# Performance work log

Hardware: AMD Instinct MI355X
Metric: run time of the kernel (lower is better)

## Reference

```python
import jax, jax.numpy as jnp
import numpy as np

GROUP = 64   # quantization group size (nunchaku W4A4 default)
QMAX = 7.0   # symmetric int4 positive range


def setup_inputs() -> dict:
    key = jax.random.key(0)
    ks = jax.random.split(key, 6)
    T, K, N, R = 256, 3072, 3072, 32
    x = jax.random.normal(ks[0], (T, K), dtype=jnp.float32)
    # int4 weight codes stored as 0..15 (dequant subtracts zero-point 8)
    qweight = jax.random.randint(ks[1], (N, K), 0, 16, dtype=jnp.int32)
    # per-(out_channel, input_group) weight scales, small positive
    wscales = jax.random.uniform(ks[2], (N, K // GROUP), dtype=jnp.float32) * 0.02 + 1e-3
    lora_down = jax.random.normal(ks[3], (R, K), dtype=jnp.float32) / np.sqrt(K)
    lora_up = jax.random.normal(ks[4], (N, R), dtype=jnp.float32) / np.sqrt(R)
    bias = jax.random.normal(ks[5], (N,), dtype=jnp.float32) * 0.01
    return {"x": x, "qweight": qweight, "wscales": wscales,
            "lora_down": lora_down, "lora_up": lora_up, "bias": bias}


def _quantize_act(x):
    # per-token, per-group symmetric int4 fake-quant (quantize -> dequantize)
    T, K = x.shape
    xg = x.reshape(T, K // GROUP, GROUP)
    scale = jnp.maximum(jnp.max(jnp.abs(xg), axis=-1, keepdims=True) / QMAX, 1e-8)
    q = jnp.clip(jnp.round(xg / scale), -8.0, QMAX)
    return (q * scale).reshape(T, K)


def reference(x, qweight, wscales, lora_down, lora_up, bias):
    # Dequantize int4 weights: (code - 8) * per-group scale  -> [N, K]
    N, K = qweight.shape
    w = (qweight.astype(jnp.float32) - 8.0).reshape(N, K // GROUP, GROUP)
    w = (w * wscales[:, :, None]).reshape(N, K)
    # W4A4 main path: int4-quantized activations x dequantized int4 weights
    x_dq = _quantize_act(x)
    main = x_dq @ w.T                               # [T, N]
    # fused low-rank (SVDQuant LoRA) branch on full-precision activations
    lora = (x @ lora_down.T) @ lora_up.T            # [T, R] @ [R, N]
    return main + lora + bias
```

## Files before the change

kernel.cpp:

```cpp
#include <hip/hip_runtime.h>
#include <stdint.h>

#define T_DIM 256
#define K_DIM 3072
#define N_DIM 3072
#define R_DIM 32
#define KG    48
#define NSPLIT 6

#define QA_BLOCKS 3072
#define LM_BLOCKS 96
#define BO_BLOCKS 768

typedef __bf16 bf16x8 __attribute__((ext_vector_type(8)));
typedef float  f32x4  __attribute__((ext_vector_type(4)));
typedef unsigned short u16x8 __attribute__((ext_vector_type(8)));

__device__ __forceinline__ unsigned short f2bf(float f) {
    unsigned u = __builtin_bit_cast(unsigned, f);
    unsigned rounding = 0x7FFFu + ((u >> 16) & 1u);
    return (unsigned short)((u + rounding) >> 16);
}

__device__ __forceinline__ bf16x8 cvt8(const float* p) {
    float4 lo = ((const float4*)p)[0], hi = ((const float4*)p)[1];
    bf16x8 v;
    v[0] = (__bf16)lo.x; v[1] = (__bf16)lo.y; v[2] = (__bf16)lo.z; v[3] = (__bf16)lo.w;
    v[4] = (__bf16)hi.x; v[5] = (__bf16)hi.y; v[6] = (__bf16)hi.z; v[7] = (__bf16)hi.w;
    return v;
}

__global__ __launch_bounds__(256) void prep(
        const float* __restrict__ x,
        const float* __restrict__ lora_down,
        const float* __restrict__ bias,
        unsigned short* __restrict__ Ap,
        float*          __restrict__ Lm,
        float*          __restrict__ out) {
    int blk = blockIdx.x;
    if (blk < QA_BLOCKS) {
        int widx = blk * 4 + (threadIdx.x >> 6);
        int lane = threadIdx.x & 63;
        int t = widx / KG, g = widx % KG;
        float v = x[(size_t)t * K_DIM + g * 64 + lane];
        float a = fabsf(v);
        #pragma unroll
        for (int off = 32; off; off >>= 1) a = fmaxf(a, __shfl_xor(a, off));
        float scale = fmaxf(a / 7.0f, 1e-8f);
        float q = rintf(v / scale);
        q = fminf(fmaxf(q, -8.f), 7.f);
        Ap[(((size_t)g * 8 + (lane >> 3)) * 256 + t) * 8 + (lane & 7)] = f2bf(q * scale);
    } else if (blk < QA_BLOCKS + LM_BLOCKS) {
        int kb = blk - QA_BLOCKS;
        int lane = threadIdx.x & 63, wv = threadIdx.x >> 6;
        int mrow = lane & 15, quad = lane >> 4;
        int k0 = kb * 32 + quad * 8;
        bf16x8 a[4], b[2];
        #pragma unroll
        for (int mt = 0; mt < 4; ++mt)
            a[mt] = cvt8(x + (size_t)(wv * 64 + mt * 16 + mrow) * K_DIM + k0);
        #pragma unroll
        for (int nt = 0; nt < 2; ++nt)
            b[nt] = cvt8(lora_down + (size_t)(nt * 16 + mrow) * K_DIM + k0);
        f32x4 acc[4][2];
        f32x4 zero = {0.f, 0.f, 0.f, 0.f};
        #pragma unroll
        for (int i = 0; i < 4; ++i) { acc[i][0] = zero; acc[i][1] = zero; }
        #pragma unroll
        for (int mt = 0; mt < 4; ++mt)
            #pragma unroll
            for (int nt = 0; nt < 2; ++nt)
                acc[mt][nt] = __builtin_amdgcn_mfma_f32_16x16x32_bf16(
                    a[mt], b[nt], acc[mt][nt], 0, 0, 0);
        #pragma unroll
        for (int mt = 0; mt < 4; ++mt)
            #pragma unroll
            for (int nt = 0; nt < 2; ++nt)
                #pragma unroll
                for (int r = 0; r < 4; ++r)
                    atomicAdd(&Lm[(size_t)(wv * 64 + mt * 16 + quad * 4 + r) * R_DIM
                                  + nt * 16 + mrow], acc[mt][nt][r]);
    } else {
        int i = (blk - QA_BLOCKS - LM_BLOCKS) * 256 + threadIdx.x;
        float4 bv = *(const float4*)&bias[(i * 4) % N_DIM];
        ((float4*)out)[i] = bv;
    }
}

__global__ __launch_bounds__(256) void gemm_main(
        const uint4*    __restrict__ ApU,
        const int*      __restrict__ qweight,
        const float*    __restrict__ wscales,
        const float*    __restrict__ Lm,
        const float*    __restrict__ lora_up,
        float*          __restrict__ out) {
    __shared__ uint4 BsU[2][512];
    int nblk  = blockIdx.x;
    int mblk  = blockIdx.y;
    int split = blockIdx.z;
    int c0 = split * (KG / NSPLIT);
    int c1 = (split == NSPLIT - 1) ? KG + 1 : c0 + (KG / NSPLIT);
    int tid = threadIdx.x;
    int lane = tid & 63, wv = tid >> 6;
    int mrow = lane & 15, quad = lane >> 4;
    int n_row = tid >> 2, seg = tid & 3;
    const int nbase = nblk * 64;
    const int mbase = mblk * 128 + wv * 32;

    f32x4 acc[2][4];
    f32x4 zero = {0.f, 0.f, 0.f, 0.f};
    #pragma unroll
    for (int i = 0; i < 2; ++i)
        #pragma unroll
        for (int j = 0; j < 4; ++j) acc[i][j] = zero;

    int4  qc[2][4];
    float wsr[2];
    bf16x8 af[2][2][2];

    const float* wsrow = wscales + (size_t)(nbase + n_row) * KG;
    const int4* qrow = (const int4*)(qweight + (size_t)(nbase + n_row) * K_DIM + seg * 16);

    #define AFRAG(kt, ks, mt) \
        (*(const bf16x8*)&ApU[(size_t)(kt) * 2048 + ((ks) * 4 + quad) * 256 + \
                              mbase + (mt) * 16 + mrow])

    {
        #pragma unroll
        for (int ks = 0; ks < 2; ++ks)
            #pragma unroll
            for (int mt = 0; mt < 2; ++mt)
                af[0][ks][mt] = AFRAG(c0, ks, mt);
        #pragma unroll
        for (int j = 0; j < 4; ++j) {
            qc[0][j] = qrow[(size_t)c0 * 16 + j];
            qc[1][j] = qrow[(size_t)(c0 + 1) * 16 + j];
        }
        wsr[0] = wsrow[c0];
        wsr[1] = wsrow[c0 + 1];
    }

    #define STEP(PP, KT)                                                          \
    {                                                                             \
        constexpr int p = (PP);                                                   \
        const int kk = (KT);                                                      \
        if (kk < KG) {                                                            \
            float w = wsr[p];                                                     \
            float m8w = -8.0f * w;                                                \
            int4 ca = qc[p][0], cb = qc[p][1], cc = qc[p][2], cd = qc[p][3];      \
            bf16x8 v0, v1;                                                        \
            v0[0] = (__bf16)__builtin_fmaf((float)ca.x, w, m8w);                  \
            v0[1] = (__bf16)__builtin_fmaf((float)ca.y, w, m8w);                  \
            v0[2] = (__bf16)__builtin_fmaf((float)ca.z, w, m8w);                  \
            v0[3] = (__bf16)__builtin_fmaf((float)ca.w, w, m8w);                  \
            v0[4] = (__bf16)__builtin_fmaf((float)cb.x, w, m8w);                  \
            v0[5] = (__bf16)__builtin_fmaf((float)cb.y, w, m8w);                  \
            v0[6] = (__bf16)__builtin_fmaf((float)cb.z, w, m8w);                  \
            v0[7] = (__bf16)__builtin_fmaf((float)cb.w, w, m8w);                  \
            v1[0] = (__bf16)__builtin_fmaf((float)cc.x, w, m8w);                  \
            v1[1] = (__bf16)__builtin_fmaf((float)cc.y, w, m8w);                  \
            v1[2] = (__bf16)__builtin_fmaf((float)cc.z, w, m8w);                  \
            v1[3] = (__bf16)__builtin_fmaf((float)cc.w, w, m8w);                  \
            v1[4] = (__bf16)__builtin_fmaf((float)cd.x, w, m8w);                  \
            v1[5] = (__bf16)__builtin_fmaf((float)cd.y, w, m8w);                  \
            v1[6] = (__bf16)__builtin_fmaf((float)cd.z, w, m8w);                  \
            v1[7] = (__bf16)__builtin_fmaf((float)cd.w, w, m8w);                  \
            BsU[p][(seg * 2 + 0) * 64 + n_row] = __builtin_bit_cast(uint4, v0);   \
            BsU[p][(seg * 2 + 1) * 64 + n_row] = __builtin_bit_cast(uint4, v1);   \
        } else {                                                                  \
            bf16x8 v0 = __builtin_bit_cast(bf16x8, (u16x8)(0));                   \
            bf16x8 v1 = __builtin_bit_cast(bf16x8, (u16x8)(0));                   \
            if (seg < 2) {                                                        \
                const float* lu = lora_up + (size_t)(nbase + n_row) * R_DIM + seg * 16; \
                _Pragma("unroll")                                                 \
                for (int j = 0; j < 8; ++j) {                                     \
                    v0[j] = (__bf16)lu[j];                                        \
                    v1[j] = (__bf16)lu[8 + j];                                    \
                }                                                                 \
            }                                                                     \
            BsU[p][(seg * 2 + 0) * 64 + n_row] = __builtin_bit_cast(uint4, v0);   \
            BsU[p][(seg * 2 + 1) * 64 + n_row] = __builtin_bit_cast(uint4, v1);   \
        }                                                                         \
        __syncthreads();                                                          \
        if (kk + 2 < c1 && kk + 2 < KG) {                                         \
            _Pragma("unroll")                                                     \
            for (int j = 0; j < 4; ++j)                                           \
                qc[p][j] = qrow[(size_t)(kk + 2) * 16 + j];                       \
            wsr[p] = wsrow[kk + 2];                                               \
        }                                                                         \
        if (kk + 1 < c1) {                                                        \
            if (kk + 1 < KG) {                                                    \
                _Pragma("unroll")                                                 \
                for (int ks = 0; ks < 2; ++ks)                                    \
                    _Pragma("unroll")                                             \
                    for (int mt = 0; mt < 2; ++mt)                                \
                        af[p ^ 1][ks][mt] = AFRAG(kk + 1, ks, mt);                \
            } else {                                                              \
                _Pragma("unroll")                                                 \
                for (int mt = 0; mt < 2; ++mt) {                                  \
                    int row = mbase + mt * 16 + mrow;                             \
                    if (quad < 4)                                                 \
                        af[p ^ 1][0][mt] = cvt8(Lm + (size_t)row * R_DIM + quad * 8); \
                    else                                                          \
                        af[p ^ 1][0][mt] = __builtin_bit_cast(bf16x8, (u16x8)(0)); \
                    af[p ^ 1][1][mt] = __builtin_bit_cast(bf16x8, (u16x8)(0));    \
                }                                                                 \
            }                                                                     \
        }                                                                         \
        _Pragma("unroll")                                                         \
        for (int ks = 0; ks < 2; ++ks) {                                          \
            bf16x8 b[4];                                                          \
            _Pragma("unroll")                                                     \
            for (int nt = 0; nt < 4; ++nt) {                                      \
                uint4 tb = BsU[p][(ks * 4 + quad) * 64 + nt * 16 + mrow];         \
                b[nt] = __builtin_bit_cast(bf16x8, tb);                           \
            }                                                                     \
            _Pragma("unroll")                                                     \
            for (int mt = 0; mt < 2; ++mt)                                        \
                _Pragma("unroll")                                                 \
                for (int nt = 0; nt < 4; ++nt)                                    \
                    acc[mt][nt] = __builtin_amdgcn_mfma_f32_16x16x32_bf16(        \
                        af[p][ks][mt], b[nt], acc[mt][nt], 0, 0, 0);              \
        }                                                                         \
    }

    int kt = c0;
    for (; kt + 1 < c1; kt += 2) {
        STEP(0, kt);
        STEP(1, kt + 1);
    }
    if (kt < c1) STEP(0, kt);

    #undef STEP
    #undef AFRAG
    #pragma unroll
    for (int nt = 0; nt < 4; ++nt) {
        int n = nbase + nt * 16 + mrow;
        #pragma unroll
        for (int mt = 0; mt < 2; ++mt) {
            int row0 = mblk * 128 + wv * 32 + mt * 16 + quad * 4;
            #pragma unroll
            for (int r = 0; r < 4; ++r)
                atomicAdd(&out[(size_t)(row0 + r) * N_DIM + n], acc[mt][nt][r]);
        }
    }
}

extern "C" void kernel_launch(void* const* d_in, const int* in_sizes, int n_in,
                              void* d_out, int out_size, void* d_ws, size_t ws_size,
                              hipStream_t stream) {
    const float* x         = (const float*)d_in[0];
    const int*   qweight   = (const int*)d_in[1];
    const float* wscales   = (const float*)d_in[2];
    const float* lora_down = (const float*)d_in[3];
    const float* lora_up   = (const float*)d_in[4];
    const float* bias      = (const float*)d_in[5];

    char* wsp = (char*)d_ws;
    unsigned short* Ap = (unsigned short*)wsp;
    wsp += (size_t)KG * 2048 * 16;
    float* Lm = (float*)wsp;

    hipMemsetAsync(Lm, 0, (size_t)T_DIM * R_DIM * sizeof(float), stream);
    prep<<<QA_BLOCKS + LM_BLOCKS + BO_BLOCKS, 256, 0, stream>>>(
        x, lora_down, bias, Ap, Lm, (float*)d_out);
    gemm_main<<<dim3(48, 2, NSPLIT), 256, 0, stream>>>(
        (const uint4*)Ap, qweight, wscales, Lm, lora_up, (float*)d_out);
}
```

Before: 116.5 us.

## Cover all tokens per block to dequantize each weight tile once

Drops the M-dimension block split so each block's four waves cover all 256 tokens, 64 rows per wave with a 4x4 accumulator tile. NSPLIT doubles so the grid stays the same size. Each int4 weight tile, stored as int32 codes, is now loaded and dequantized once instead of twice, which halves qweight traffic and dequant ALU work. In exchange, the A-fragment double-buffer prefetch is removed, so activation fragments are loaded within each step with less latency hiding, register pressure rises, and each split covers fewer K groups.

```diff
diff --git a/kernel.cpp b/kernel.cpp
--- a/kernel.cpp
+++ b/kernel.cpp
@@ -6,7 +6,7 @@
 #define N_DIM 3072
 #define R_DIM 32
 #define KG    48
-#define NSPLIT 6
+#define NSPLIT 12
 
 #define QA_BLOCKS 3072
 #define LM_BLOCKS 96
@@ -96,8 +96,7 @@
         float*          __restrict__ out) {
     __shared__ uint4 BsU[2][512];
     int nblk  = blockIdx.x;
-    int mblk  = blockIdx.y;
-    int split = blockIdx.z;
+    int split = blockIdx.y;
     int c0 = split * (KG / NSPLIT);
     int c1 = (split == NSPLIT - 1) ? KG + 1 : c0 + (KG / NSPLIT);
     int tid = threadIdx.x;
@@ -105,18 +104,17 @@
     int mrow = lane & 15, quad = lane >> 4;
     int n_row = tid >> 2, seg = tid & 3;
     const int nbase = nblk * 64;
-    const int mbase = mblk * 128 + wv * 32;
-
-    f32x4 acc[2][4];
+    const int mbase = wv * 64;
+
+    f32x4 acc[4][4];
     f32x4 zero = {0.f, 0.f, 0.f, 0.f};
     #pragma unroll
-    for (int i = 0; i < 2; ++i)
+    for (int i = 0; i < 4; ++i)
         #pragma unroll
         for (int j = 0; j < 4; ++j) acc[i][j] = zero;
 
     int4  qc[2][4];
     float wsr[2];
-    bf16x8 af[2][2][2];
 
     const float* wsrow = wscales + (size_t)(nbase + n_row) * KG;
     const int4* qrow = (const int4*)(qweight + (size_t)(nbase + n_row) * K_DIM + seg * 16);
@@ -126,11 +124,6 @@
                               mbase + (mt) * 16 + mrow])
 
     {
-        #pragma unroll
-        for (int ks = 0; ks < 2; ++ks)
-            #pragma unroll
-            for (int mt = 0; mt < 2; ++mt)
-                af[0][ks][mt] = AFRAG(c0, ks, mt);
         #pragma unroll
         for (int j = 0; j < 4; ++j) {
             qc[0][j] = qrow[(size_t)c0 * 16 + j];
@@ -188,23 +181,19 @@
                 qc[p][j] = qrow[(size_t)(kk + 2) * 16 + j];                       \
             wsr[p] = wsrow[kk + 2];                                               \
         }                                                                         \
-        if (kk + 1 < c1) {                                                        \
-            if (kk + 1 < KG) {                                                    \
+        bf16x8 afc[2][4];                                                         \
+        if (kk < KG) {                                                            \
+            _Pragma("unroll")                                                     \
+            for (int ks = 0; ks < 2; ++ks)                                        \
                 _Pragma("unroll")                                                 \
-                for (int ks = 0; ks < 2; ++ks)                                    \
-                    _Pragma("unroll")                                             \
-                    for (int mt = 0; mt < 2; ++mt)                                \
-                        af[p ^ 1][ks][mt] = AFRAG(kk + 1, ks, mt);                \
-            } else {                                                              \
-                _Pragma("unroll")                                                 \
-                for (int mt = 0; mt < 2; ++mt) {                                  \
-                    int row = mbase + mt * 16 + mrow;                             \
-                    if (quad < 4)                                                 \
-                        af[p ^ 1][0][mt] = cvt8(Lm + (size_t)row * R_DIM + quad * 8); \
-                    else                                                          \
-                        af[p ^ 1][0][mt] = __builtin_bit_cast(bf16x8, (u16x8)(0)); \
-                    af[p ^ 1][1][mt] = __builtin_bit_cast(bf16x8, (u16x8)(0));    \
-                }                                                                 \
+                for (int mt = 0; mt < 4; ++mt)                                    \
+                    afc[ks][mt] = AFRAG(kk, ks, mt);                              \
+        } else {                                                                  \
+            _Pragma("unroll")                                                     \
+            for (int mt = 0; mt < 4; ++mt) {                                      \
+                int row = mbase + mt * 16 + mrow;                                 \
+                afc[0][mt] = cvt8(Lm + (size_t)row * R_DIM + quad * 8);           \
+                afc[1][mt] = __builtin_bit_cast(bf16x8, (u16x8)(0));              \
             }                                                                     \
         }                                                                         \
         _Pragma("unroll")                                                         \
@@ -216,11 +205,11 @@
                 b[nt] = __builtin_bit_cast(bf16x8, tb);                           \
             }                                                                     \
             _Pragma("unroll")                                                     \
-            for (int mt = 0; mt < 2; ++mt)                                        \
+            for (int mt = 0; mt < 4; ++mt)                                        \
                 _Pragma("unroll")                                                 \
                 for (int nt = 0; nt < 4; ++nt)                                    \
                     acc[mt][nt] = __builtin_amdgcn_mfma_f32_16x16x32_bf16(        \
-                        af[p][ks][mt], b[nt], acc[mt][nt], 0, 0, 0);              \
+                        afc[ks][mt], b[nt], acc[mt][nt], 0, 0, 0);                \
         }                                                                         \
     }
 
@@ -237,8 +226,8 @@
     for (int nt = 0; nt < 4; ++nt) {
         int n = nbase + nt * 16 + mrow;
         #pragma unroll
-        for (int mt = 0; mt < 2; ++mt) {
-            int row0 = mblk * 128 + wv * 32 + mt * 16 + quad * 4;
+        for (int mt = 0; mt < 4; ++mt) {
+            int row0 = mbase + mt * 16 + quad * 4;
             #pragma unroll
             for (int r = 0; r < 4; ++r)
                 atomicAdd(&out[(size_t)(row0 + r) * N_DIM + n], acc[mt][nt][r]);
@@ -264,6 +253,6 @@
     hipMemsetAsync(Lm, 0, (size_t)T_DIM * R_DIM * sizeof(float), stream);
     prep<<<QA_BLOCKS + LM_BLOCKS + BO_BLOCKS, 256, 0, stream>>>(
         x, lora_down, bias, Ap, Lm, (float*)d_out);
-    gemm_main<<<dim3(48, 2, NSPLIT), 256, 0, stream>>>(
+    gemm_main<<<dim3(48, NSPLIT), 256, 0, stream>>>(
         (const uint4*)Ap, qweight, wscales, Lm, lora_up, (float*)d_out);
 }
```

Measured after the change: 128.3 us. +10.2%, slower.
